# Performance work log

Measured on AMD Instinct MI355X. Metric: run time of the kernel, lower is better.

## Reference

```python
import jax, jax.numpy as jnp
import numpy as np


def _relative_position_index(w):
    # Deterministic Swin relative-position index, shape [w*w, w*w], values in [0, (2w-1)^2)
    coords_h = np.arange(w)
    coords_w = np.arange(w)
    coords = np.stack(np.meshgrid(coords_h, coords_w, indexing="ij"))  # [2, w, w]
    coords = coords.reshape(2, -1)                                      # [2, w*w]
    rel = coords[:, :, None] - coords[:, None, :]                       # [2, N, N]
    rel = rel.transpose(1, 2, 0).copy()                                 # [N, N, 2]
    rel[:, :, 0] += w - 1
    rel[:, :, 1] += w - 1
    rel[:, :, 0] *= 2 * w - 1
    return jnp.asarray(rel.sum(-1), dtype=jnp.int32)


def setup_inputs() -> dict:
    key = jax.random.key(0)
    ks = jax.random.split(key, 7)
    BS, N, C, H, W = 4096, 49, 384, 12, 7
    NW = 64  # number of windows per image
    x = jax.random.normal(ks[0], (BS, N, C), dtype=jnp.float32)
    # Swin shift mask: 0 where attention allowed, -100 where blocked
    u = jax.random.uniform(ks[1], (NW, N, N))
    mask = jnp.where(u < 0.5, 0.0, -100.0).astype(jnp.float32)
    qkv_w = jax.random.normal(ks[2], (C, 3 * C), dtype=jnp.float32) * (C ** -0.5)
    qkv_b = jax.random.normal(ks[3], (3 * C,), dtype=jnp.float32) * 0.02
    proj_w = jax.random.normal(ks[4], (C, C), dtype=jnp.float32) * (C ** -0.5)
    proj_b = jax.random.normal(ks[5], (C,), dtype=jnp.float32) * 0.02
    bias_table = jax.random.normal(ks[6], ((2 * W - 1) ** 2, H), dtype=jnp.float32) * 0.02
    return {"x": x, "mask": mask, "qkv_w": qkv_w, "qkv_b": qkv_b,
            "proj_w": proj_w, "proj_b": proj_b, "bias_table": bias_table,
            "n_heads": 12, "window_size": 7}


def reference(x, mask, qkv_w, qkv_b, proj_w, proj_b, bias_table, n_heads, window_size):
    BS, N, C = x.shape
    Hh = n_heads
    hd = C // Hh
    scale = hd ** -0.5
    rpi = _relative_position_index(window_size)  # [N, N] int

    qkv = x @ qkv_w + qkv_b                       # [BS, N, 3C]
    qkv = qkv.reshape(BS, N, 3, Hh, hd).transpose(2, 0, 3, 1, 4)  # [3, BS, H, N, hd]
    q, k, v = qkv[0], qkv[1], qkv[2]

    attn = jnp.einsum("bhnd,bhmd->bhnm", q, k) * scale   # [BS, H, N, N]
    # relative position bias gather: [N*N, H] -> [H, N, N]
    rpb = bias_table[rpi.reshape(-1)].reshape(N, N, Hh).transpose(2, 0, 1)
    attn = attn + rpb[None]

    nw = mask.shape[0]
    attn = attn.reshape(BS // nw, nw, Hh, N, N) + mask[None, :, None]
    attn = attn.reshape(BS, Hh, N, N)

    attn = jax.nn.softmax(attn, axis=-1)
    out = jnp.einsum("bhnm,bhmd->bhnd", attn, v)          # [BS, H, N, hd]
    out = out.transpose(0, 2, 1, 3).reshape(BS, N, C)
    return out @ proj_w + proj_b
```

## Files before the change

kernel.cpp:

```cpp
#include <hip/hip_runtime.h>
#include <hip/hip_bf16.h>


typedef __attribute__((ext_vector_type(8))) short bf16x8;
typedef __attribute__((ext_vector_type(4))) float f32x4;

#define SEQ_N  49
#define CH     384
#define QKV_N  1152
#define UNIT_ROWS 3136
#define BM2_ELEMS (64 * 12 * 49 * 64)

__device__ __forceinline__ unsigned short f2b(float f) {
    union { float f; unsigned int u; } v; v.f = f;
    return (unsigned short)((v.u + 0x7FFFu + ((v.u >> 16) & 1u)) >> 16);
}

__device__ __forceinline__ bf16x8 ld8(const unsigned short* p) {
    return *(const bf16x8*)p;
}

__device__ __forceinline__ void gload16(const unsigned short* g, unsigned short* l) {
    __builtin_amdgcn_global_load_lds(
        (const __attribute__((address_space(1))) unsigned int*)g,
        (__attribute__((address_space(3))) unsigned int*)l, 16, 0, 0);
}

__device__ __forceinline__ int xcd_swizzle(int orig, int T) {
    int q = T >> 3, r = T & 7;
    int xcd = orig & 7, idx = orig >> 3;
    return (xcd < r ? xcd * (q + 1) : r * (q + 1) + (xcd - r) * q) + idx;
}

__global__ __launch_bounds__(256) void k_cvt_w(const float* __restrict__ wq,
        const float* __restrict__ wp, unsigned short* __restrict__ oq,
        unsigned short* __restrict__ op)
{
    int t = blockIdx.x * 256 + threadIdx.x;
    if (t < QKV_N * CH) {
        int n = t / CH, k = t - n * CH;
        oq[t] = f2b(wq[(size_t)k * QKV_N + n]);
    }
    if (t < CH * CH) {
        int n = t / CH, k = t - n * CH;
        op[t] = f2b(wp[(size_t)k * CH + n]);
    }
}

__global__ __launch_bounds__(256) void k_bm(const float* __restrict__ btab,
        const float* __restrict__ mask, float* __restrict__ bm2)
{
    int t = blockIdx.x * 256 + threadIdx.x;
    if (t >= BM2_ELEMS) return;
    int w    = t / (12 * 49 * 64);
    int rem  = t - w * 12 * 49 * 64;
    int h    = rem / (49 * 64);
    int rem2 = rem - h * 49 * 64;
    int i    = rem2 >> 6;
    int s    = rem2 & 63;
    int j15  = s >> 2, nt = s & 3;
    int j    = nt * 16 + j15;
    float v = -1e30f;
    if (j < 49) {
        int ih = i / 7, iw = i - (i / 7) * 7;
        int jh = j / 7, jw = j - (j / 7) * 7;
        int idx = (ih - jh + 6) * 13 + (iw - jw + 6);
        v = btab[idx * 12 + h] + mask[(size_t)w * 2401 + i * 49 + j];
    }
    bm2[t] = v;
}

__global__ __launch_bounds__(256) void k_cvt(const float* __restrict__ in,
        unsigned short* __restrict__ outp, int n8)
{
    int stride = gridDim.x * 256;
    for (int i = blockIdx.x * 256 + threadIdx.x; i < n8; i += stride) {
        const float4* p = (const float4*)(in + (size_t)i * 8);
        float4 a = p[0], b = p[1];
        uint4 v;
        v.x = (unsigned)f2b(a.x) | ((unsigned)f2b(a.y) << 16);
        v.y = (unsigned)f2b(a.z) | ((unsigned)f2b(a.w) << 16);
        v.z = (unsigned)f2b(b.x) | ((unsigned)f2b(b.y) << 16);
        v.w = (unsigned)f2b(b.z) | ((unsigned)f2b(b.w) << 16);
        *(uint4*)(outp + (size_t)i * 8) = v;
    }
}

template<int OUTF32>
__global__ __launch_bounds__(512, 6) void k_gemm(
        const unsigned short* __restrict__ A, int lda,
        const unsigned short* __restrict__ Bt, int K,
        const float* __restrict__ bias,
        unsigned short* __restrict__ Cb, float* __restrict__ Cf, int ldc,
        int M, int ntiles, int mtiles)
{
    __shared__ unsigned short As[3 * 4096];
    __shared__ unsigned short Bs[3 * 4096];
    const int wg = xcd_swizzle(blockIdx.x, mtiles * ntiles);
    const int m0 = (wg / ntiles) * 128;
    const int n0 = (wg % ntiles) * 128;
    const int tid = threadIdx.x;
    const int lane = tid & 63, wv = tid >> 6;
    const int wr = wv >> 2, wc = wv & 3;
    const int l15 = lane & 15, g = lane >> 4;

    f32x4 acc[4][2];
#pragma unroll
    for (int a = 0; a < 4; ++a)
#pragma unroll
        for (int b = 0; b < 2; ++b) acc[a][b] = (f32x4){0.f, 0.f, 0.f, 0.f};

    int arow = m0 + (tid >> 2); if (arow > M - 1) arow = M - 1;
    const unsigned short* aP = A + (size_t)arow * lda + (tid & 3) * 8;
    const unsigned short* bP = Bt + (size_t)(n0 + (tid >> 2)) * K + (tid & 3) * 8;
    const int lo = wv * 512;

#define STAGE(kt, buf) do {                                \
        gload16(aP + (kt), &As[(buf) * 4096 + lo]);        \
        gload16(bP + (kt), &Bs[(buf) * 4096 + lo]);        \
    } while (0)

#define COMPUTE(buf) do {                                                       \
        bf16x8 af[4], bfr[2];                                                   \
        _Pragma("unroll")                                                       \
        for (int mt = 0; mt < 4; ++mt)                                          \
            af[mt] = ld8(&As[(buf) * 4096 + (wr * 64 + mt * 16 + l15) * 32 + g * 8]); \
        _Pragma("unroll")                                                       \
        for (int nt = 0; nt < 2; ++nt)                                          \
            bfr[nt] = ld8(&Bs[(buf) * 4096 + (wc * 32 + nt * 16 + l15) * 32 + g * 8]); \
        __builtin_amdgcn_s_setprio(1);                                          \
        _Pragma("unroll")                                                       \
        for (int mt = 0; mt < 4; ++mt)                                          \
            _Pragma("unroll")                                                   \
            for (int nt = 0; nt < 2; ++nt)                                      \
                acc[mt][nt] = __builtin_amdgcn_mfma_f32_16x16x32_bf16(          \
                        af[mt], bfr[nt], acc[mt][nt], 0, 0, 0);                 \
        __builtin_amdgcn_s_setprio(0);                                          \
    } while (0)

    const int nsteps = K >> 5;

    STAGE(0, 0);
    STAGE(32, 1);

    int cur = 0;
    for (int t = 0; t < nsteps - 2; ++t) {
        int pf = cur + 2; if (pf >= 3) pf -= 3;
        STAGE((t + 2) * 32, pf);
        __builtin_amdgcn_sched_barrier(0);
        asm volatile("s_waitcnt vmcnt(4)" ::: "memory");
        __builtin_amdgcn_sched_barrier(0);
        __builtin_amdgcn_s_barrier();
        __builtin_amdgcn_sched_barrier(0);
        COMPUTE(cur);
        __builtin_amdgcn_sched_barrier(0);
        __builtin_amdgcn_s_barrier();
        __builtin_amdgcn_sched_barrier(0);
        cur = (cur == 2) ? 0 : cur + 1;
    }
    asm volatile("s_waitcnt vmcnt(2)" ::: "memory");
    __builtin_amdgcn_sched_barrier(0);
    __builtin_amdgcn_s_barrier();
    __builtin_amdgcn_sched_barrier(0);
    COMPUTE(cur);
    __builtin_amdgcn_sched_barrier(0);
    __builtin_amdgcn_s_barrier();
    __builtin_amdgcn_sched_barrier(0);
    cur = (cur == 2) ? 0 : cur + 1;
    asm volatile("s_waitcnt vmcnt(0)" ::: "memory");
    __builtin_amdgcn_sched_barrier(0);
    __builtin_amdgcn_s_barrier();
    __builtin_amdgcn_sched_barrier(0);
    COMPUTE(cur);
#undef STAGE
#undef COMPUTE

#pragma unroll
    for (int mt = 0; mt < 4; ++mt)
#pragma unroll
        for (int nt = 0; nt < 2; ++nt) {
            int col = n0 + wc * 32 + nt * 16 + l15;
            float bb = bias[col];
#pragma unroll
            for (int r = 0; r < 4; ++r) {
                int row = m0 + wr * 64 + mt * 16 + g * 4 + r;
                if (row < M) {
                    if (OUTF32)
                        Cf[(size_t)row * ldc + col] = acc[mt][nt][r] + bb;
                    else
                        Cb[(size_t)row * ldc + col] = f2b(acc[mt][nt][r] + bb);
                }
            }
        }
}

__global__ __launch_bounds__(256) void k_attn(unsigned short* __restrict__ qkv,
        const float* __restrict__ bm2)
{
    extern __shared__ unsigned short sm[];
    const int tid = threadIdx.x;
    const int lane = tid & 63, wv = tid >> 6;
    const int l15 = lane & 15, g = lane >> 4;
    const int pair = blockIdx.x * 4 + wv;
    const int winloc = pair / 12;
    const int h = pair - winloc * 12;
    const int wimg = winloc & 63;
    const int co = h * 32;
    unsigned short* Vt = sm + wv * 6048;
    unsigned short* Pw = Vt + 32 * 72;
    unsigned short* src = qkv + (size_t)winloc * SEQ_N * QKV_N;
    const float* bm2h = bm2 + ((size_t)(wimg * 12 + h)) * (49 * 64);

    for (int t = lane; t < 32 * 16; t += 64) {
        int c = t >> 4, kk = 48 + (t & 15);
        Vt[c * 72 + kk] = 0;
    }
    for (int t = lane; t < 49 * 4; t += 64) {
        int row = t >> 2, cb = (t & 3) * 8;
        const unsigned short* vp = src + (size_t)row * QKV_N + 768 + co + cb;
        ushort4 a = ((const ushort4*)vp)[0];
        ushort4 b = ((const ushort4*)vp)[1];
        Vt[(cb + 0) * 72 + row] = a.x; Vt[(cb + 1) * 72 + row] = a.y;
        Vt[(cb + 2) * 72 + row] = a.z; Vt[(cb + 3) * 72 + row] = a.w;
        Vt[(cb + 4) * 72 + row] = b.x; Vt[(cb + 5) * 72 + row] = b.y;
        Vt[(cb + 6) * 72 + row] = b.z; Vt[(cb + 7) * 72 + row] = b.w;
    }

    bf16x8 qf[4], kf[4];
#pragma unroll
    for (int mt = 0; mt < 4; ++mt) {
        int r = mt * 16 + l15; if (r > 48) r = 48;
        qf[mt] = ld8(src + (size_t)r * QKV_N + co + g * 8);
    }
#pragma unroll
    for (int nt = 0; nt < 4; ++nt) {
        int r = nt * 16 + l15; if (r > 48) r = 48;
        kf[nt] = ld8(src + (size_t)r * QKV_N + CH + co + g * 8);
    }

    f32x4 sa[4][4];
#pragma unroll
    for (int mt = 0; mt < 4; ++mt)
#pragma unroll
        for (int nt = 0; nt < 4; ++nt) sa[mt][nt] = (f32x4){0.f, 0.f, 0.f, 0.f};
#pragma unroll
    for (int mt = 0; mt < 4; ++mt)
#pragma unroll
        for (int nt = 0; nt < 4; ++nt)
            sa[mt][nt] = __builtin_amdgcn_mfma_f32_16x16x32_bf16(
                    qf[mt], kf[nt], sa[mt][nt], 0, 0, 0);

    const float scale = 0.17677669529663687f;
#pragma unroll
    for (int mt = 0; mt < 4; ++mt) {
#pragma unroll
        for (int r = 0; r < 4; ++r) {
            int i = mt * 16 + g * 4 + r;
            int ic = i < 49 ? i : 48;
            float4 bv = *(const float4*)(bm2h + (size_t)ic * 64 + l15 * 4);
            float sv[4];
            sv[0] = sa[mt][0][r] * scale + bv.x;
            sv[1] = sa[mt][1][r] * scale + bv.y;
            sv[2] = sa[mt][2][r] * scale + bv.z;
            sv[3] = sa[mt][3][r] * scale + bv.w;
            float mx = fmaxf(fmaxf(sv[0], sv[1]), fmaxf(sv[2], sv[3]));
#pragma unroll
            for (int d = 1; d < 16; d <<= 1) mx = fmaxf(mx, __shfl_xor(mx, d));
            float sum = 0.f;
#pragma unroll
            for (int nt = 0; nt < 4; ++nt) { sv[nt] = __expf(sv[nt] - mx); sum += sv[nt]; }
#pragma unroll
            for (int d = 1; d < 16; d <<= 1) sum += __shfl_xor(sum, d);
            float inv = 1.0f / sum;
            if (i < 52) {
#pragma unroll
                for (int nt = 0; nt < 4; ++nt)
                    Pw[i * 72 + nt * 16 + l15] = f2b(sv[nt] * inv);
            }
        }
    }
    __syncthreads();

    f32x4 oa[4][2];
#pragma unroll
    for (int mt = 0; mt < 4; ++mt)
#pragma unroll
        for (int nt = 0; nt < 2; ++nt) oa[mt][nt] = (f32x4){0.f, 0.f, 0.f, 0.f};
#pragma unroll
    for (int ks = 0; ks < 2; ++ks) {
        bf16x8 pf[4];
#pragma unroll
        for (int mt = 0; mt < 4; ++mt) {
            int pr = mt * 16 + l15; if (pr > 51) pr = 51;
            pf[mt] = ld8(Pw + pr * 72 + ks * 32 + g * 8);
        }
#pragma unroll
        for (int nt = 0; nt < 2; ++nt) {
            bf16x8 vf = ld8(Vt + (nt * 16 + l15) * 72 + ks * 32 + g * 8);
#pragma unroll
            for (int mt = 0; mt < 4; ++mt)
                oa[mt][nt] = __builtin_amdgcn_mfma_f32_16x16x32_bf16(
                        pf[mt], vf, oa[mt][nt], 0, 0, 0);
        }
    }

#pragma unroll
    for (int mt = 0; mt < 4; ++mt)
#pragma unroll
        for (int r = 0; r < 4; ++r) {
            int i = mt * 16 + g * 4 + r;
            if (i < 49) {
#pragma unroll
                for (int nt = 0; nt < 2; ++nt)
                    src[(size_t)i * QKV_N + co + nt * 16 + l15] = f2b(oa[mt][nt][r]);
            }
        }
}

extern "C" void kernel_launch(void* const* d_in, const int* in_sizes, int n_in,
                              void* d_out, int out_size, void* d_ws, size_t ws_size,
                              hipStream_t stream) {
    const float* x      = (const float*)d_in[0];
    const float* mask   = (const float*)d_in[1];
    const float* qkv_w  = (const float*)d_in[2];
    const float* qkv_b  = (const float*)d_in[3];
    const float* proj_w = (const float*)d_in[4];
    const float* proj_b = (const float*)d_in[5];
    const float* btab   = (const float*)d_in[6];
    float* out = (float*)d_out;

    unsigned short* wq_bt = (unsigned short*)d_ws;
    unsigned short* wp_bt = wq_bt + QKV_N * CH;
    float*          bm2   = (float*)(wp_bt + CH * CH);
    unsigned short* base  = (unsigned short*)(bm2 + BM2_ELEMS);
    const size_t fixed = (size_t)(QKV_N * CH + CH * CH) * 2 + (size_t)BM2_ELEMS * 4;
    const size_t unit  = (size_t)UNIT_ROWS * (CH + QKV_N) * 2;
    if (ws_size < fixed + unit) return;
    int upc = (int)((ws_size - fixed) / unit);
    if (upc > 64) upc = 64;
    unsigned short* xb  = base;
    unsigned short* qkv = base + (size_t)upc * UNIT_ROWS * CH;

    const int smem2 = 4 * 6048 * 2;
    hipFuncSetAttribute(reinterpret_cast<const void*>(k_attn),
                        hipFuncAttributeMaxDynamicSharedMemorySize, smem2);

    dim3 blk(256);
    k_cvt_w<<<dim3((QKV_N * CH + 255) / 256), blk, 0, stream>>>(qkv_w, proj_w, wq_bt, wp_bt);
    k_bm   <<<dim3((BM2_ELEMS + 255) / 256), blk, 0, stream>>>(btab, mask, bm2);

    for (int u0 = 0; u0 < 64; u0 += upc) {
        int units = (64 - u0) < upc ? (64 - u0) : upc;
        int m_base = u0 * UNIT_ROWS;
        int Mc = units * UNIT_ROWS;
        int mtiles = (Mc + 127) / 128;
        k_cvt<<<dim3(2048), blk, 0, stream>>>(x + (size_t)m_base * CH, xb, Mc * 48);
        k_gemm<0><<<dim3(mtiles * 9), dim3(512), 0, stream>>>(
                xb, CH, wq_bt, CH, qkv_b, qkv, nullptr, QKV_N, Mc, 9, mtiles);
        k_attn<<<dim3(units * 192), blk, smem2, stream>>>(qkv, bm2);
        k_gemm<1><<<dim3(mtiles * 3), dim3(512), 0, stream>>>(
                qkv, QKV_N, wp_bt, CH, proj_b, nullptr, out + (size_t)m_base * CH,
                CH, Mc, 3, mtiles);
    }
}
```

Before: 863.1 us.

## Fuse fp32-to-bf16 conversion of x into the QKV GEMM A-tile loads

Removes the separate k_cvt pass and the bf16 copy of x. The new QKV GEMM reads fp32 x directly, converts it in registers and writes bf16 into a double-buffered, swizzled LDS A tile, while B keeps its async global-to-LDS triple buffering. This avoids writing and re-reading a bf16 activation buffer and one kernel launch. In exchange, each x element is fetched once per N tile (nine times) as fp32, and the register-staged path adds conversion work and waits inside the GEMM main loop.

```diff
diff --git a/kernel.cpp b/kernel.cpp
--- a/kernel.cpp
+++ b/kernel.cpp
@@ -70,28 +70,124 @@
     bm2[t] = v;
 }
 
-__global__ __launch_bounds__(256) void k_cvt(const float* __restrict__ in,
-        unsigned short* __restrict__ outp, int n8)
+__global__ __launch_bounds__(512, 6) void k_qkvx(
+        const float* __restrict__ X,
+        const unsigned short* __restrict__ Bt,
+        const float* __restrict__ bias,
+        unsigned short* __restrict__ C, int M, int mtiles)
 {
-    int stride = gridDim.x * 256;
-    for (int i = blockIdx.x * 256 + threadIdx.x; i < n8; i += stride) {
-        const float4* p = (const float4*)(in + (size_t)i * 8);
-        float4 a = p[0], b = p[1];
-        uint4 v;
-        v.x = (unsigned)f2b(a.x) | ((unsigned)f2b(a.y) << 16);
-        v.y = (unsigned)f2b(a.z) | ((unsigned)f2b(a.w) << 16);
-        v.z = (unsigned)f2b(b.x) | ((unsigned)f2b(b.y) << 16);
-        v.w = (unsigned)f2b(b.z) | ((unsigned)f2b(b.w) << 16);
-        *(uint4*)(outp + (size_t)i * 8) = v;
-    }
-}
-
-template<int OUTF32>
-__global__ __launch_bounds__(512, 6) void k_gemm(
+    __shared__ unsigned short As[2 * 4096];
+    __shared__ unsigned short Bs[3 * 4096];
+    const int wg = xcd_swizzle(blockIdx.x, mtiles * 9);
+    const int m0 = (wg / 9) * 128;
+    const int n0 = (wg % 9) * 128;
+    const int tid = threadIdx.x;
+    const int lane = tid & 63, wv = tid >> 6;
+    const int wr = wv >> 2, wc = wv & 3;
+    const int l15 = lane & 15, g = lane >> 4;
+
+    f32x4 acc[4][2];
+#pragma unroll
+    for (int a = 0; a < 4; ++a)
+#pragma unroll
+        for (int b = 0; b < 2; ++b) acc[a][b] = (f32x4){0.f, 0.f, 0.f, 0.f};
+
+    const int ar = tid >> 2, lc = tid & 3;
+    int arow = m0 + ar; if (arow > M - 1) arow = M - 1;
+    const float* xP = X + (size_t)arow * CH + lc * 8;
+    unsigned short* aW0 = As + ar * 32 + ((lc ^ (ar & 3)) * 8);
+    const unsigned short* bP = Bt + (size_t)(n0 + ar) * CH + lc * 8;
+    const int lo = wv * 512;
+
+#define GB(kt, buf)  gload16(bP + (kt), &Bs[(buf) * 4096 + lo])
+
+#define COMPUTE(ta, tb) do {                                                    \
+        const unsigned short* pa = As + ((ta) & 1) * 4096;                      \
+        const unsigned short* pb = &Bs[((tb) % 3) * 4096];                      \
+        bf16x8 af[4], bfr[2];                                                   \
+        _Pragma("unroll")                                                       \
+        for (int mt = 0; mt < 4; ++mt) {                                        \
+            int row = wr * 64 + mt * 16 + l15;                                  \
+            af[mt] = ld8(pa + row * 32 + ((g ^ (row & 3)) * 8));                \
+        }                                                                       \
+        _Pragma("unroll")                                                       \
+        for (int nt = 0; nt < 2; ++nt)                                          \
+            bfr[nt] = ld8(pb + (wc * 32 + nt * 16 + l15) * 32 + g * 8);         \
+        __builtin_amdgcn_s_setprio(1);                                          \
+        _Pragma("unroll")                                                       \
+        for (int mt = 0; mt < 4; ++mt)                                          \
+            _Pragma("unroll")                                                   \
+            for (int nt = 0; nt < 2; ++nt)                                      \
+                acc[mt][nt] = __builtin_amdgcn_mfma_f32_16x16x32_bf16(          \
+                        af[mt], bfr[nt], acc[mt][nt], 0, 0, 0);                 \
+        __builtin_amdgcn_s_setprio(0);                                          \
+    } while (0)
+
+    const int ns = 12;
+
+    {
+        float4 p0 = *(const float4*)(xP);
+        float4 p1 = *(const float4*)(xP + 4);
+        GB(0, 0);
+        GB(32, 1);
+        bf16x8 w8;
+        w8[0] = (short)f2b(p0.x); w8[1] = (short)f2b(p0.y);
+        w8[2] = (short)f2b(p0.z); w8[3] = (short)f2b(p0.w);
+        w8[4] = (short)f2b(p1.x); w8[5] = (short)f2b(p1.y);
+        w8[6] = (short)f2b(p1.z); w8[7] = (short)f2b(p1.w);
+        *(bf16x8*)aW0 = w8;
+        asm volatile("s_waitcnt vmcnt(1)" ::: "memory");
+        asm volatile("s_waitcnt lgkmcnt(0)" ::: "memory");
+        __builtin_amdgcn_s_barrier();
+        __builtin_amdgcn_sched_barrier(0);
+    }
+
+    for (int t = 0; t < ns; ++t) {
+        float4 p0, p1;
+        if (t + 1 < ns) {
+            p0 = *(const float4*)(xP + (t + 1) * 32);
+            p1 = *(const float4*)(xP + (t + 1) * 32 + 4);
+        }
+        if (t + 2 < ns) GB((t + 2) * 32, (t + 2) % 3);
+        __builtin_amdgcn_sched_barrier(0);
+        COMPUTE(t, t);
+        if (t + 1 < ns) {
+            if (t + 2 < ns) asm volatile("s_waitcnt vmcnt(1)" ::: "memory");
+            else            asm volatile("s_waitcnt vmcnt(0)" ::: "memory");
+            __builtin_amdgcn_sched_barrier(0);
+            bf16x8 w8;
+            w8[0] = (short)f2b(p0.x); w8[1] = (short)f2b(p0.y);
+            w8[2] = (short)f2b(p0.z); w8[3] = (short)f2b(p0.w);
+            w8[4] = (short)f2b(p1.x); w8[5] = (short)f2b(p1.y);
+            w8[6] = (short)f2b(p1.z); w8[7] = (short)f2b(p1.w);
+            *(bf16x8*)(As + ((t + 1) & 1) * 4096 + ar * 32 + ((lc ^ (ar & 3)) * 8)) = w8;
+            asm volatile("s_waitcnt lgkmcnt(0)" ::: "memory");
+            __builtin_amdgcn_s_barrier();
+            __builtin_amdgcn_sched_barrier(0);
+        }
+    }
+#undef GB
+#undef COMPUTE
+
+#pragma unroll
+    for (int mt = 0; mt < 4; ++mt)
+#pragma unroll
+        for (int nt = 0; nt < 2; ++nt) {
+            int col = n0 + wc * 32 + nt * 16 + l15;
+            float bb = bias[col];
+#pragma unroll
+            for (int r = 0; r < 4; ++r) {
+                int row = m0 + wr * 64 + mt * 16 + g * 4 + r;
+                if (row < M)
+                    C[(size_t)row * QKV_N + col] = f2b(acc[mt][nt][r] + bb);
+            }
+        }
+}
+
+__global__ __launch_bounds__(512, 6) void k_proj(
         const unsigned short* __restrict__ A, int lda,
         const unsigned short* __restrict__ Bt, int K,
-        const float* __restrict__ bias,
-        unsigned short* __restrict__ Cb, float* __restrict__ Cf, int ldc,
+        const float* __restrict__ bias, float* __restrict__ Cf, int ldc,
         int M, int ntiles, int mtiles)
 {
     __shared__ unsigned short As[3 * 4096];
@@ -184,12 +280,8 @@
 #pragma unroll
             for (int r = 0; r < 4; ++r) {
                 int row = m0 + wr * 64 + mt * 16 + g * 4 + r;
-                if (row < M) {
-                    if (OUTF32)
-                        Cf[(size_t)row * ldc + col] = acc[mt][nt][r] + bb;
-                    else
-                        Cb[(size_t)row * ldc + col] = f2b(acc[mt][nt][r] + bb);
-                }
+                if (row < M)
+                    Cf[(size_t)row * ldc + col] = acc[mt][nt][r] + bb;
             }
         }
 }
@@ -332,14 +424,12 @@
     unsigned short* wq_bt = (unsigned short*)d_ws;
     unsigned short* wp_bt = wq_bt + QKV_N * CH;
     float*          bm2   = (float*)(wp_bt + CH * CH);
-    unsigned short* base  = (unsigned short*)(bm2 + BM2_ELEMS);
+    unsigned short* qkv   = (unsigned short*)(bm2 + BM2_ELEMS);
     const size_t fixed = (size_t)(QKV_N * CH + CH * CH) * 2 + (size_t)BM2_ELEMS * 4;
-    const size_t unit  = (size_t)UNIT_ROWS * (CH + QKV_N) * 2;
+    const size_t unit  = (size_t)UNIT_ROWS * QKV_N * 2;
     if (ws_size < fixed + unit) return;
     int upc = (int)((ws_size - fixed) / unit);
     if (upc > 64) upc = 64;
-    unsigned short* xb  = base;
-    unsigned short* qkv = base + (size_t)upc * UNIT_ROWS * CH;
 
     const int smem2 = 4 * 6048 * 2;
     hipFuncSetAttribute(reinterpret_cast<const void*>(k_attn),
@@ -354,12 +444,11 @@
         int m_base = u0 * UNIT_ROWS;
         int Mc = units * UNIT_ROWS;
         int mtiles = (Mc + 127) / 128;
-        k_cvt<<<dim3(2048), blk, 0, stream>>>(x + (size_t)m_base * CH, xb, Mc * 48);
-        k_gemm<0><<<dim3(mtiles * 9), dim3(512), 0, stream>>>(
-                xb, CH, wq_bt, CH, qkv_b, qkv, nullptr, QKV_N, Mc, 9, mtiles);
+        k_qkvx<<<dim3(mtiles * 9), dim3(512), 0, stream>>>(
+                x + (size_t)m_base * CH, wq_bt, qkv_b, qkv, Mc, mtiles);
         k_attn<<<dim3(units * 192), blk, smem2, stream>>>(qkv, bm2);
-        k_gemm<1><<<dim3(mtiles * 3), dim3(512), 0, stream>>>(
-                qkv, QKV_N, wp_bt, CH, proj_b, nullptr, out + (size_t)m_base * CH,
+        k_proj<<<dim3(mtiles * 3), dim3(512), 0, stream>>>(
+                qkv, QKV_N, wp_bt, CH, proj_b, out + (size_t)m_base * CH,
                 CH, Mc, 3, mtiles);
     }
 }
```

After: 865.2 us. About the same (+0.2%).

## Switch GEMM to double-buffered 64-wide K tiles instead of triple-buffered 32-wide

Applied to the files above, without the earlier changes.

The GEMM k-loop now stages 64-element K slices (four global-to-LDS loads per thread) into two buffers instead of 32-element slices into three buffers. This halves the number of loop iterations and the barriers between them, and each barrier interval now covers twice the MFMA work. In exchange the prefetch depth drops from two stages to one, LDS use per block grows from 48KB to 64KB, and the occupancy hint is lowered from 6 to 4, so less latency hiding is available.

```diff
diff --git a/kernel.cpp b/kernel.cpp
--- a/kernel.cpp
+++ b/kernel.cpp
@@ -87,15 +87,15 @@
 }
 
 template<int OUTF32>
-__global__ __launch_bounds__(512, 6) void k_gemm(
+__global__ __launch_bounds__(512, 4) void k_gemm(
         const unsigned short* __restrict__ A, int lda,
         const unsigned short* __restrict__ Bt, int K,
         const float* __restrict__ bias,
         unsigned short* __restrict__ Cb, float* __restrict__ Cf, int ldc,
         int M, int ntiles, int mtiles)
 {
-    __shared__ unsigned short As[3 * 4096];
-    __shared__ unsigned short Bs[3 * 4096];
+    __shared__ unsigned short As[2 * 8192];
+    __shared__ unsigned short Bs[2 * 8192];
     const int wg = xcd_swizzle(blockIdx.x, mtiles * ntiles);
     const int m0 = (wg / ntiles) * 128;
     const int n0 = (wg % ntiles) * 128;
@@ -110,68 +110,66 @@
 #pragma unroll
         for (int b = 0; b < 2; ++b) acc[a][b] = (f32x4){0.f, 0.f, 0.f, 0.f};
 
-    int arow = m0 + (tid >> 2); if (arow > M - 1) arow = M - 1;
-    const unsigned short* aP = A + (size_t)arow * lda + (tid & 3) * 8;
-    const unsigned short* bP = Bt + (size_t)(n0 + (tid >> 2)) * K + (tid & 3) * 8;
+    const int srow = tid >> 3, sch = (tid & 7) * 8;
+    int ra0 = m0 + srow;       if (ra0 > M - 1) ra0 = M - 1;
+    int ra1 = m0 + 64 + srow;  if (ra1 > M - 1) ra1 = M - 1;
+    const unsigned short* a0p = A + (size_t)ra0 * lda + sch;
+    const unsigned short* a1p = A + (size_t)ra1 * lda + sch;
+    const unsigned short* b0p = Bt + (size_t)(n0 + srow) * K + sch;
+    const unsigned short* b1p = Bt + (size_t)(n0 + 64 + srow) * K + sch;
     const int lo = wv * 512;
 
-#define STAGE(kt, buf) do {                                \
-        gload16(aP + (kt), &As[(buf) * 4096 + lo]);        \
-        gload16(bP + (kt), &Bs[(buf) * 4096 + lo]);        \
+#define STAGE(kt, buf) do {                                   \
+        gload16(a0p + (kt), &As[(buf) * 8192 + lo]);          \
+        gload16(a1p + (kt), &As[(buf) * 8192 + 4096 + lo]);   \
+        gload16(b0p + (kt), &Bs[(buf) * 8192 + lo]);          \
+        gload16(b1p + (kt), &Bs[(buf) * 8192 + 4096 + lo]);   \
     } while (0)
 
 #define COMPUTE(buf) do {                                                       \
-        bf16x8 af[4], bfr[2];                                                   \
         _Pragma("unroll")                                                       \
-        for (int mt = 0; mt < 4; ++mt)                                          \
-            af[mt] = ld8(&As[(buf) * 4096 + (wr * 64 + mt * 16 + l15) * 32 + g * 8]); \
-        _Pragma("unroll")                                                       \
-        for (int nt = 0; nt < 2; ++nt)                                          \
-            bfr[nt] = ld8(&Bs[(buf) * 4096 + (wc * 32 + nt * 16 + l15) * 32 + g * 8]); \
-        __builtin_amdgcn_s_setprio(1);                                          \
-        _Pragma("unroll")                                                       \
-        for (int mt = 0; mt < 4; ++mt)                                          \
+        for (int kh = 0; kh < 2; ++kh) {                                        \
+            bf16x8 af[4], bfr[2];                                               \
+            _Pragma("unroll")                                                   \
+            for (int mt = 0; mt < 4; ++mt)                                      \
+                af[mt] = ld8(&As[(buf) * 8192 + (wr * 64 + mt * 16 + l15) * 64  \
+                                 + kh * 32 + g * 8]);                           \
             _Pragma("unroll")                                                   \
             for (int nt = 0; nt < 2; ++nt)                                      \
-                acc[mt][nt] = __builtin_amdgcn_mfma_f32_16x16x32_bf16(          \
-                        af[mt], bfr[nt], acc[mt][nt], 0, 0, 0);                 \
-        __builtin_amdgcn_s_setprio(0);                                          \
+                bfr[nt] = ld8(&Bs[(buf) * 8192 + (wc * 32 + nt * 16 + l15) * 64 \
+                                  + kh * 32 + g * 8]);                          \
+            __builtin_amdgcn_s_setprio(1);                                      \
+            _Pragma("unroll")                                                   \
+            for (int mt = 0; mt < 4; ++mt)                                      \
+                _Pragma("unroll")                                               \
+                for (int nt = 0; nt < 2; ++nt)                                  \
+                    acc[mt][nt] = __builtin_amdgcn_mfma_f32_16x16x32_bf16(      \
+                            af[mt], bfr[nt], acc[mt][nt], 0, 0, 0);             \
+            __builtin_amdgcn_s_setprio(0);                                      \
+        }                                                                       \
     } while (0)
 
-    const int nsteps = K >> 5;
+    const int nsteps = K >> 6;
 
     STAGE(0, 0);
-    STAGE(32, 1);
-
-    int cur = 0;
-    for (int t = 0; t < nsteps - 2; ++t) {
-        int pf = cur + 2; if (pf >= 3) pf -= 3;
-        STAGE((t + 2) * 32, pf);
-        __builtin_amdgcn_sched_barrier(0);
-        asm volatile("s_waitcnt vmcnt(4)" ::: "memory");
+
+    for (int t = 0; t < nsteps; ++t) {
+        if (t + 1 < nsteps) {
+            STAGE((t + 1) * 64, (t + 1) & 1);
+            __builtin_amdgcn_sched_barrier(0);
+            asm volatile("s_waitcnt vmcnt(4)" ::: "memory");
+        } else {
+            __builtin_amdgcn_sched_barrier(0);
+            asm volatile("s_waitcnt vmcnt(0)" ::: "memory");
+        }
         __builtin_amdgcn_sched_barrier(0);
         __builtin_amdgcn_s_barrier();
         __builtin_amdgcn_sched_barrier(0);
-        COMPUTE(cur);
+        COMPUTE(t & 1);
         __builtin_amdgcn_sched_barrier(0);
         __builtin_amdgcn_s_barrier();
         __builtin_amdgcn_sched_barrier(0);
-        cur = (cur == 2) ? 0 : cur + 1;
-    }
-    asm volatile("s_waitcnt vmcnt(2)" ::: "memory");
-    __builtin_amdgcn_sched_barrier(0);
-    __builtin_amdgcn_s_barrier();
-    __builtin_amdgcn_sched_barrier(0);
-    COMPUTE(cur);
-    __builtin_amdgcn_sched_barrier(0);
-    __builtin_amdgcn_s_barrier();
-    __builtin_amdgcn_sched_barrier(0);
-    cur = (cur == 2) ? 0 : cur + 1;
-    asm volatile("s_waitcnt vmcnt(0)" ::: "memory");
-    __builtin_amdgcn_sched_barrier(0);
-    __builtin_amdgcn_s_barrier();
-    __builtin_amdgcn_sched_barrier(0);
-    COMPUTE(cur);
+    }
 #undef STAGE
 #undef COMPUTE
 
```

After: 963.0 us. 11.6% more time.
